# Optimization experiments

Hardware: AMD Instinct MI355X
Metric: run time of the kernel (lower is better)

Reference implementation:

```python
import jax, jax.numpy as jnp
import numpy as np


def setup_inputs() -> dict:
    key = jax.random.key(0)
    x = jax.random.normal(key, (4096, 512), dtype=jnp.float32)
    return {"x": x}


def reference(x):
    # Pairwise Euclidean distances for all (i, j) with i > j, flattened in the
    # same order as the original nested loop: (1,0),(2,0),(2,1),(3,0),...
    n = x.shape[0]
    sq = jnp.sum(x * x, axis=1)                      # [N]
    gram = x @ x.T                                   # [N, N]
    d2 = sq[:, None] + sq[None, :] - 2.0 * gram      # [N, N] squared dists
    ii, jj = jnp.tril_indices(n, k=-1)               # row-major lower triangle
    return jnp.sqrt(jnp.maximum(d2[ii, jj], 0.0))    # [N*(N-1)/2]
```

## Files before the change

### kernel.cpp

```cpp
#include <hip/hip_runtime.h>
#include <hip/hip_bf16.h>
#include <stdint.h>

#define N 4096
#define D 512
#define TILE 128
#define BK 32
#define NB (N / TILE)

typedef __bf16 bf16x8 __attribute__((ext_vector_type(8)));
typedef float f32x4 __attribute__((ext_vector_type(4)));

__global__ __launch_bounds__(256) void prep_kernel(const float* __restrict__ x,
                                                   __bf16* __restrict__ xb,
                                                   float* __restrict__ sq) {
    int row  = blockIdx.x * 4 + (threadIdx.x >> 6);
    int lane = threadIdx.x & 63;
    const float* xr = x + (size_t)row * D + lane * 8;
    float4 v0 = *reinterpret_cast<const float4*>(xr);
    float4 v1 = *reinterpret_cast<const float4*>(xr + 4);

    bf16x8 b;
    b[0] = (__bf16)v0.x; b[1] = (__bf16)v0.y; b[2] = (__bf16)v0.z; b[3] = (__bf16)v0.w;
    b[4] = (__bf16)v1.x; b[5] = (__bf16)v1.y; b[6] = (__bf16)v1.z; b[7] = (__bf16)v1.w;
    *reinterpret_cast<bf16x8*>(xb + (size_t)row * D + lane * 8) = b;

    float s = v0.x * v0.x + v0.y * v0.y + v0.z * v0.z + v0.w * v0.w +
              v1.x * v1.x + v1.y * v1.y + v1.z * v1.z + v1.w * v1.w;
    #pragma unroll
    for (int off = 32; off > 0; off >>= 1) s += __shfl_down(s, off);
    if (lane == 0) sq[row] = s;
}

__global__ __launch_bounds__(256) void pairdist_kernel(const __bf16* __restrict__ xb,
                                                       const float* __restrict__ sq,
                                                       float* __restrict__ out) {
    __shared__ __bf16 As[TILE * BK];
    __shared__ __bf16 Bs[TILE * BK];

    int t  = blockIdx.x;
    int bi = (int)((sqrtf(8.0f * (float)t + 1.0f) - 1.0f) * 0.5f);
    while ((bi + 1) * (bi + 2) / 2 <= t) bi++;
    while (bi * (bi + 1) / 2 > t) bi--;
    int bj = t - bi * (bi + 1) / 2;

    int tid  = threadIdx.x;
    int w    = tid >> 6;
    int lane = tid & 63;
    int quad = lane >> 4;
    int lr   = lane & 15;
    int wm   = w >> 1;
    int wn   = w & 1;

    f32x4 acc[4][4];
    #pragma unroll
    for (int mt = 0; mt < 4; mt++)
        #pragma unroll
        for (int nt = 0; nt < 4; nt++)
            acc[mt][nt] = (f32x4)0.0f;

    int srow = lane >> 2;
    int scol = (lane & 3) * 8;
    const __bf16* ga = xb + (size_t)(bi * TILE + w * 16 + srow) * D + scol;
    const __bf16* gb = xb + (size_t)(bj * TILE + w * 16 + srow) * D + scol;
    __bf16* la = As + w * 16 * BK;
    __bf16* lb = Bs + w * 16 * BK;

    for (int k0 = 0; k0 < D; k0 += BK) {
        __syncthreads();
        __builtin_amdgcn_global_load_lds(
            (const __attribute__((address_space(1))) void*)(ga + k0),
            (__attribute__((address_space(3))) void*)la, 16, 0, 0);
        __builtin_amdgcn_global_load_lds(
            (const __attribute__((address_space(1))) void*)(ga + k0 + (size_t)64 * D),
            (__attribute__((address_space(3))) void*)(la + 64 * BK), 16, 0, 0);
        __builtin_amdgcn_global_load_lds(
            (const __attribute__((address_space(1))) void*)(gb + k0),
            (__attribute__((address_space(3))) void*)lb, 16, 0, 0);
        __builtin_amdgcn_global_load_lds(
            (const __attribute__((address_space(1))) void*)(gb + k0 + (size_t)64 * D),
            (__attribute__((address_space(3))) void*)(lb + 64 * BK), 16, 0, 0);
        __syncthreads();

        bf16x8 af[4], bfr[4];
        #pragma unroll
        for (int mt = 0; mt < 4; mt++)
            af[mt] = *reinterpret_cast<const bf16x8*>(
                As + (wm * 64 + mt * 16 + lr) * BK + quad * 8);
        #pragma unroll
        for (int nt = 0; nt < 4; nt++)
            bfr[nt] = *reinterpret_cast<const bf16x8*>(
                Bs + (wn * 64 + nt * 16 + lr) * BK + quad * 8);

        #pragma unroll
        for (int mt = 0; mt < 4; mt++)
            #pragma unroll
            for (int nt = 0; nt < 4; nt++)
                acc[mt][nt] = __builtin_amdgcn_mfma_f32_16x16x32_bf16(
                    af[mt], bfr[nt], acc[mt][nt], 0, 0, 0);
    }

    int ibase = bi * TILE + wm * 64;
    int jbase = bj * TILE + wn * 64;

    float sqi[4][4], sqj[4];
    #pragma unroll
    for (int mt = 0; mt < 4; mt++)
        #pragma unroll
        for (int tt = 0; tt < 4; tt++)
            sqi[mt][tt] = sq[ibase + mt * 16 + quad * 4 + tt];
    #pragma unroll
    for (int nt = 0; nt < 4; nt++)
        sqj[nt] = sq[jbase + nt * 16 + lr];

    #pragma unroll
    for (int mt = 0; mt < 4; mt++) {
        #pragma unroll
        for (int tt = 0; tt < 4; tt++) {
            int i = ibase + mt * 16 + quad * 4 + tt;
            unsigned rowoff = (unsigned)(i * (i - 1) / 2);
            #pragma unroll
            for (int nt = 0; nt < 4; nt++) {
                int j = jbase + nt * 16 + lr;
                if (j < i) {
                    float d2 = sqi[mt][tt] + sqj[nt] - 2.0f * acc[mt][nt][tt];
                    out[rowoff + (unsigned)j] = sqrtf(fmaxf(d2, 0.0f));
                }
            }
        }
    }
}

extern "C" void kernel_launch(void* const* d_in, const int* in_sizes, int n_in,
                              void* d_out, int out_size, void* d_ws, size_t ws_size,
                              hipStream_t stream) {
    const float* x = (const float*)d_in[0];
    float* out = (float*)d_out;

    __bf16* xb = (__bf16*)d_ws;
    float* sq  = (float*)((char*)d_ws + (size_t)N * D * sizeof(__bf16));

    prep_kernel<<<N / 4, 256, 0, stream>>>(x, xb, sq);

    int nblocks = NB * (NB + 1) / 2;
    pairdist_kernel<<<nblocks, 256, 0, stream>>>(xb, sq, out);
}
```

Measured before the change: 89.43 us.

## Double-buffer LDS tiles and drop bounds checks for off-diagonal blocks

Adds a second LDS buffer for the A and B tiles. The next K-slice is issued with global_load_lds while MFMAs run on the current slice, which cuts the per-iteration sync from two barriers to one. The epilogue is also split so off-diagonal blocks store without the j<i check. The change doubles LDS use to 32KB per block, which may lower occupancy. The single barrier assumes the async LDS loads have completed by the next iteration, and it is unclear whether the compiler inserts the needed vmcnt wait.

```diff
diff --git a/kernel.cpp b/kernel.cpp
--- a/kernel.cpp
+++ b/kernel.cpp
@@ -6,6 +6,7 @@
 #define D 512
 #define TILE 128
 #define BK 32
+#define KITERS (D / BK)
 #define NB (N / TILE)
 
 typedef __bf16 bf16x8 __attribute__((ext_vector_type(8)));
@@ -35,8 +36,8 @@
 __global__ __launch_bounds__(256) void pairdist_kernel(const __bf16* __restrict__ xb,
                                                        const float* __restrict__ sq,
                                                        float* __restrict__ out) {
-    __shared__ __bf16 As[TILE * BK];
-    __shared__ __bf16 Bs[TILE * BK];
+    __shared__ __bf16 As[2][TILE * BK];
+    __shared__ __bf16 Bs[2][TILE * BK];
 
     int t  = blockIdx.x;
     int bi = (int)((sqrtf(8.0f * (float)t + 1.0f) - 1.0f) * 0.5f);
@@ -63,34 +64,44 @@
     int scol = (lane & 3) * 8;
     const __bf16* ga = xb + (size_t)(bi * TILE + w * 16 + srow) * D + scol;
     const __bf16* gb = xb + (size_t)(bj * TILE + w * 16 + srow) * D + scol;
-    __bf16* la = As + w * 16 * BK;
-    __bf16* lb = Bs + w * 16 * BK;
+    int ldsoff = w * 16 * BK;
 
-    for (int k0 = 0; k0 < D; k0 += BK) {
-        __syncthreads();
-        __builtin_amdgcn_global_load_lds(
-            (const __attribute__((address_space(1))) void*)(ga + k0),
-            (__attribute__((address_space(3))) void*)la, 16, 0, 0);
-        __builtin_amdgcn_global_load_lds(
-            (const __attribute__((address_space(1))) void*)(ga + k0 + (size_t)64 * D),
-            (__attribute__((address_space(3))) void*)(la + 64 * BK), 16, 0, 0);
-        __builtin_amdgcn_global_load_lds(
-            (const __attribute__((address_space(1))) void*)(gb + k0),
-            (__attribute__((address_space(3))) void*)lb, 16, 0, 0);
-        __builtin_amdgcn_global_load_lds(
-            (const __attribute__((address_space(1))) void*)(gb + k0 + (size_t)64 * D),
-            (__attribute__((address_space(3))) void*)(lb + 64 * BK), 16, 0, 0);
-        __syncthreads();
+#define STAGE(buf, k0)                                                        \
+    do {                                                                      \
+        __builtin_amdgcn_global_load_lds(                                     \
+            (const __attribute__((address_space(1))) void*)(ga + (k0)),       \
+            (__attribute__((address_space(3))) void*)(As[buf] + ldsoff),      \
+            16, 0, 0);                                                        \
+        __builtin_amdgcn_global_load_lds(                                     \
+            (const __attribute__((address_space(1))) void*)(ga + (k0) + (size_t)64 * D), \
+            (__attribute__((address_space(3))) void*)(As[buf] + ldsoff + 64 * BK), \
+            16, 0, 0);                                                        \
+        __builtin_amdgcn_global_load_lds(                                     \
+            (const __attribute__((address_space(1))) void*)(gb + (k0)),       \
+            (__attribute__((address_space(3))) void*)(Bs[buf] + ldsoff),      \
+            16, 0, 0);                                                        \
+        __builtin_amdgcn_global_load_lds(                                     \
+            (const __attribute__((address_space(1))) void*)(gb + (k0) + (size_t)64 * D), \
+            (__attribute__((address_space(3))) void*)(Bs[buf] + ldsoff + 64 * BK), \
+            16, 0, 0);                                                        \
+    } while (0)
+
+    STAGE(0, 0);
+    __syncthreads();
+
+    for (int it = 0; it < KITERS; ++it) {
+        int cur = it & 1;
+        if (it + 1 < KITERS) STAGE(cur ^ 1, (it + 1) * BK);
 
         bf16x8 af[4], bfr[4];
         #pragma unroll
         for (int mt = 0; mt < 4; mt++)
             af[mt] = *reinterpret_cast<const bf16x8*>(
-                As + (wm * 64 + mt * 16 + lr) * BK + quad * 8);
+                As[cur] + (wm * 64 + mt * 16 + lr) * BK + quad * 8);
         #pragma unroll
         for (int nt = 0; nt < 4; nt++)
             bfr[nt] = *reinterpret_cast<const bf16x8*>(
-                Bs + (wn * 64 + nt * 16 + lr) * BK + quad * 8);
+                Bs[cur] + (wn * 64 + nt * 16 + lr) * BK + quad * 8);
 
         #pragma unroll
         for (int mt = 0; mt < 4; mt++)
@@ -98,7 +109,10 @@
             for (int nt = 0; nt < 4; nt++)
                 acc[mt][nt] = __builtin_amdgcn_mfma_f32_16x16x32_bf16(
                     af[mt], bfr[nt], acc[mt][nt], 0, 0, 0);
+
+        __syncthreads();
     }
+#undef STAGE
 
     int ibase = bi * TILE + wm * 64;
     int jbase = bj * TILE + wn * 64;
@@ -113,18 +127,35 @@
     for (int nt = 0; nt < 4; nt++)
         sqj[nt] = sq[jbase + nt * 16 + lr];
 
-    #pragma unroll
-    for (int mt = 0; mt < 4; mt++) {
+    if (bi != bj) {
         #pragma unroll
-        for (int tt = 0; tt < 4; tt++) {
-            int i = ibase + mt * 16 + quad * 4 + tt;
-            unsigned rowoff = (unsigned)(i * (i - 1) / 2);
+        for (int mt = 0; mt < 4; mt++) {
             #pragma unroll
-            for (int nt = 0; nt < 4; nt++) {
-                int j = jbase + nt * 16 + lr;
-                if (j < i) {
+            for (int tt = 0; tt < 4; tt++) {
+                int i = ibase + mt * 16 + quad * 4 + tt;
+                unsigned rowoff = (unsigned)(i * (i - 1) / 2);
+                #pragma unroll
+                for (int nt = 0; nt < 4; nt++) {
+                    int j = jbase + nt * 16 + lr;
                     float d2 = sqi[mt][tt] + sqj[nt] - 2.0f * acc[mt][nt][tt];
                     out[rowoff + (unsigned)j] = sqrtf(fmaxf(d2, 0.0f));
+                }
+            }
+        }
+    } else {
+        #pragma unroll
+        for (int mt = 0; mt < 4; mt++) {
+            #pragma unroll
+            for (int tt = 0; tt < 4; tt++) {
+                int i = ibase + mt * 16 + quad * 4 + tt;
+                unsigned rowoff = (unsigned)(i * (i - 1) / 2);
+                #pragma unroll
+                for (int nt = 0; nt < 4; nt++) {
+                    int j = jbase + nt * 16 + lr;
+                    if (j < i) {
+                        float d2 = sqi[mt][tt] + sqj[nt] - 2.0f * acc[mt][nt][tt];
+                        out[rowoff + (unsigned)j] = sqrtf(fmaxf(d2, 0.0f));
+                    }
                 }
             }
         }
```

Result: slower. 99.38 us (+11.1%).
